# Kernel tuning notes

Hardware: AMD Instinct MI355X
Metric: run time of the kernel (lower is better)

Reference implementation:

```python
import jax, jax.numpy as jnp
import numpy as np

GRID = 48          # static voxel-grid extent (positions generated in [0, GRID)^3)
K = 3              # kernel size per axis (odd -> offset = 0.0 in the original module)
C = (K - 1) // 2   # kernel center
VOXEL_SIZE = 1.0   # forward default in DeConvolution.call


def setup_inputs() -> dict:
    key = jax.random.key(0)
    k1, k2 = jax.random.split(key)
    g = np.arange(GRID)
    coords = np.stack(np.meshgrid(g, g, g, indexing='ij'), axis=-1).reshape(-1, 3)
    # sparse input point cloud: half-density sub-lattice; dense-ish output lattice
    inp_positions = jnp.asarray(coords[coords.sum(axis=1) % 2 == 0], jnp.float32)  # (55296, 3)
    out_positions = jnp.asarray(coords, jnp.float32)                               # (110592, 3)
    n_in = inp_positions.shape[0]
    cin, cout = 256, 256
    features = jax.random.normal(k1, (n_in, cin), dtype=jnp.float32)
    # SparseConvTranspose kernel: [k, k, k, in_channels, filters]
    W = jax.random.normal(k2, (K, K, K, cin, cout), dtype=jnp.float32) * 0.05
    return {"features": features, "inp_positions": inp_positions,
            "out_positions": out_positions, "W": W}


def reference(features, inp_positions, out_positions, W):
    # Voxelize. kernel is odd -> offset = 0.0, so v = floor(p / voxel_size).
    vin = jnp.floor(inp_positions / VOXEL_SIZE).astype(jnp.int32)   # (N_in, 3)
    vout = jnp.floor(out_positions / VOXEL_SIZE).astype(jnp.int32)  # (N_out, 3)
    n_in = features.shape[0]

    # Dense voxel -> input-row hash grid (-1 = empty voxel).
    grid = jnp.full((GRID, GRID, GRID), -1, dtype=jnp.int32)
    grid = grid.at[vin[:, 0], vin[:, 1], vin[:, 2]].set(
        jnp.arange(n_in, dtype=jnp.int32))

    out = jnp.zeros((vout.shape[0], W.shape[-1]), dtype=features.dtype)
    # Transposed sparse conv: out[j] += W[v_in - v_out + C] @ feat[i]
    # Static 27-tap loop; each tap is a gather + dense GEMM.
    for dx in range(-C, C + 1):
        for dy in range(-C, C + 1):
            for dz in range(-C, C + 1):
                u = vout + jnp.array([dx, dy, dz], dtype=jnp.int32)   # source voxel
                inb = jnp.all((u >= 0) & (u < GRID), axis=1)
                uc = jnp.clip(u, 0, GRID - 1)
                idx = grid[uc[:, 0], uc[:, 1], uc[:, 2]]              # (N_out,)
                valid = inb & (idx >= 0)
                g = jnp.where(valid[:, None],
                              features[jnp.maximum(idx, 0)], 0.0)     # (N_out, Cin)
                out = out + g @ W[dx + C, dy + C, dz + C]             # (N_out, Cout)
    return out
```

## Files before the change

kernel.cpp:

```cpp
#include <hip/hip_runtime.h>

#define NIN   55296
#define CIN   256
#define COUT  256
#define NTH   512
#define NBLK  432

typedef __attribute__((ext_vector_type(8))) _Float16 half8;
typedef __attribute__((ext_vector_type(4))) _Float16 half4;
typedef __attribute__((ext_vector_type(4))) float f32x4;

typedef const __attribute__((address_space(1))) void* gp_t;
typedef __attribute__((address_space(3))) void* lp_t;
__device__ __forceinline__ void gload16(const void* g, char* l) {
  __builtin_amdgcn_global_load_lds((gp_t)g, (lp_t)l, 16, 0, 0);
}

__global__ void k_feat_cvt(const float* __restrict__ f, _Float16* __restrict__ o, int n4) {
  int i = blockIdx.x * blockDim.x + threadIdx.x;
  if (i >= n4) return;
  f32x4 v = ((const f32x4*)f)[i];
  half4 r;
  r[0] = (_Float16)v[0]; r[1] = (_Float16)v[1];
  r[2] = (_Float16)v[2]; r[3] = (_Float16)v[3];
  ((half4*)o)[i] = r;
}

__global__ void k_w_cvt(const float* __restrict__ W, _Float16* __restrict__ Wt,
                        float* __restrict__ zeros) {
  int i = blockIdx.x * blockDim.x + threadIdx.x;
  int d   = i >> 16;
  int rem = i & 65535;
  int n   = rem >> 8;
  int k   = rem & 255;
  Wt[i] = (_Float16)W[(d << 16) + (k << 8) + n];
  if (blockIdx.x == 0 && threadIdx.x < 128) zeros[threadIdx.x] = 0.0f;
}

__global__ __launch_bounds__(NTH, 2)
void k_conv8(const _Float16* __restrict__ featb, const _Float16* __restrict__ wt,
             const char* __restrict__ zeros, float* __restrict__ out) {
  extern __shared__ char lds[];
  int* orow = (int*)(lds + 131072);

  const int braw = blockIdx.x;
  const int b    = (braw & 7) * 54 + (braw >> 3);
  const int p    = b & 1;
  const int tile = b >> 1;

  const int tid = threadIdx.x;
  const int w   = tid >> 6;
  const int l   = tid & 63;

  const int rr  = w * 16 + (l >> 2);
  const int swz = ((l & 3) ^ ((l >> 3) & 3)) * 16;

  int xs[2], ys[2], zs[2];
#pragma unroll
  for (int q = 0; q < 2; ++q) {
    int e = tile * 256 + q * 128 + rr;
    int c = e / 24;
    int zi = e - c * 24;
    int x = c / 48;
    int y = c - x * 48;
    xs[q] = x; ys[q] = y; zs[q] = 2 * zi + ((x + y + p) & 1);
  }
  const char* wtc  = (const char*)wt;
  const char* featc = (const char*)featb;
  const int bro0 = rr * 512 + swz;
  const int bro1 = (128 + rr) * 512 + swz;

  const int wm = w >> 2, wn = w & 3;
  const int lr = l & 15, kg = l >> 4;
  const int rsw = (kg ^ ((lr >> 1) & 3)) * 16;
  const int aRd = (wm * 128 + lr) * 64 + rsw;
  const int bRd = (wn * 64 + lr) * 64 + rsw;

  if (tid < 256) {
    int e = tile * 256 + tid;
    int c = e / 24;
    int zi = e - c * 24;
    int x = c / 48;
    int y = c - x * 48;
    int z = 2 * zi + ((x + y + p) & 1);
    orow[tid] = (x * 48 + y) * 48 + z;
  }

  auto offpar = [](int d) { return ((d / 9) + (d / 3) % 3 + (d % 3) + 1) & 1; };
  const char* asrc[2];
  const char* wtile;
  auto setoff = [&](int d27) {
    int dx = d27 / 9 - 1, dy = (d27 / 3) % 3 - 1, dz = d27 % 3 - 1;
#pragma unroll
    for (int q = 0; q < 2; ++q) {
      int ux = xs[q] + dx, uy = ys[q] + dy, uz = zs[q] + dz;
      bool v = (unsigned)ux < 48u && (unsigned)uy < 48u && (unsigned)uz < 48u;
      int idx = (ux * 48 + uy) * 24 + (uz >> 1);
      asrc[q] = (v ? (featc + idx * 512) : zeros) + swz;
    }
    wtile = wtc + d27 * 131072;
  };

  int pn = 0;
  while (offpar(pn) != p) ++pn;
  setoff(pn);

  gload16(asrc[0],            lds + 0     + w * 1024);
  gload16(asrc[1],            lds + 8192  + w * 1024);
  gload16(wtile + bro0,       lds + 32768 + w * 1024);
  gload16(wtile + bro1,       lds + 40960 + w * 1024);
  gload16(asrc[0] + 64,       lds + 16384 + w * 1024);
  gload16(asrc[1] + 64,       lds + 24576 + w * 1024);
  gload16(wtile + bro0 + 64,  lds + 49152 + w * 1024);
  gload16(wtile + bro1 + 64,  lds + 57344 + w * 1024);

  asm volatile("s_waitcnt lgkmcnt(0)" ::: "memory");
  asm volatile("s_waitcnt vmcnt(4)" ::: "memory");
  __builtin_amdgcn_s_barrier();

  f32x4 acc[8][4];
#pragma unroll
  for (int i = 0; i < 8; ++i)
#pragma unroll
    for (int j = 0; j < 4; ++j) acc[i][j] = (f32x4)0.0f;

  const int S = p ? 56 : 52;

#define VMC(pfv) do { if (pfv) asm volatile("s_waitcnt vmcnt(4)" ::: "memory"); \
                      else     asm volatile("s_waitcnt vmcnt(0)" ::: "memory"); } while (0)
#define PH_MID() do { __builtin_amdgcn_s_barrier(); \
                      asm volatile("s_waitcnt lgkmcnt(0)" ::: "memory"); \
                      __builtin_amdgcn_sched_barrier(0); \
                      __builtin_amdgcn_s_setprio(1); } while (0)
#define PH_END() do { __builtin_amdgcn_s_setprio(0); \
                      __builtin_amdgcn_s_barrier(); } while (0)

  for (int s = 0; s < S; ++s) {
    const int d = s & 1;
    const char* Ab = lds + d * 65536;
    const char* Bb = Ab + 32768;
    char* Nb = lds + ((d ^ 1) * 65536);
    const int  sn  = s + 1;
    const bool pf  = sn < S;
    const int  kcn = sn & 3;
    if (pf && kcn == 0) {
      do { ++pn; } while (offpar(pn) != p);
      setoff(pn);
    }
    const int kb = kcn * 128;

    half8 a0[8], a1[8], bb0, bb1;

#pragma unroll
    for (int mf = 0; mf < 8; ++mf) a0[mf] = *(const half8*)(Ab + aRd + mf * 1024);
    bb0 = *(const half8*)(Bb + bRd);
    bb1 = *(const half8*)(Bb + bRd + 1024);
    if (pf) {
      gload16(asrc[0] + kb, Nb + 0    + w * 1024);
      gload16(asrc[1] + kb, Nb + 8192 + w * 1024);
    }
    VMC(pf);
    PH_MID();
#pragma unroll
    for (int mf = 0; mf < 8; ++mf) {
      acc[mf][0] = __builtin_amdgcn_mfma_f32_16x16x32_f16(a0[mf], bb0, acc[mf][0], 0, 0, 0);
      acc[mf][1] = __builtin_amdgcn_mfma_f32_16x16x32_f16(a0[mf], bb1, acc[mf][1], 0, 0, 0);
    }
    PH_END();

    bb0 = *(const half8*)(Bb + bRd + 2048);
    bb1 = *(const half8*)(Bb + bRd + 3072);
    if (pf) {
      gload16(wtile + bro0 + kb, Nb + 32768 + w * 1024);
      gload16(wtile + bro1 + kb, Nb + 40960 + w * 1024);
    }
    VMC(pf);
    PH_MID();
#pragma unroll
    for (int mf = 0; mf < 8; ++mf) {
      acc[mf][2] = __builtin_amdgcn_mfma_f32_16x16x32_f16(a0[mf], bb0, acc[mf][2], 0, 0, 0);
      acc[mf][3] = __builtin_amdgcn_mfma_f32_16x16x32_f16(a0[mf], bb1, acc[mf][3], 0, 0, 0);
    }
    PH_END();

#pragma unroll
    for (int mf = 0; mf < 8; ++mf) a1[mf] = *(const half8*)(Ab + 16384 + aRd + mf * 1024);
    bb0 = *(const half8*)(Bb + 16384 + bRd);
    bb1 = *(const half8*)(Bb + 16384 + bRd + 1024);
    if (pf) {
      gload16(asrc[0] + kb + 64, Nb + 16384 + w * 1024);
      gload16(asrc[1] + kb + 64, Nb + 24576 + w * 1024);
    }
    VMC(pf);
    PH_MID();
#pragma unroll
    for (int mf = 0; mf < 8; ++mf) {
      acc[mf][0] = __builtin_amdgcn_mfma_f32_16x16x32_f16(a1[mf], bb0, acc[mf][0], 0, 0, 0);
      acc[mf][1] = __builtin_amdgcn_mfma_f32_16x16x32_f16(a1[mf], bb1, acc[mf][1], 0, 0, 0);
    }
    PH_END();

    bb0 = *(const half8*)(Bb + 16384 + bRd + 2048);
    bb1 = *(const half8*)(Bb + 16384 + bRd + 3072);
    if (pf) {
      gload16(wtile + bro0 + kb + 64, Nb + 49152 + w * 1024);
      gload16(wtile + bro1 + kb + 64, Nb + 57344 + w * 1024);
    }
    VMC(pf);
    PH_MID();
#pragma unroll
    for (int mf = 0; mf < 8; ++mf) {
      acc[mf][2] = __builtin_amdgcn_mfma_f32_16x16x32_f16(a1[mf], bb0, acc[mf][2], 0, 0, 0);
      acc[mf][3] = __builtin_amdgcn_mfma_f32_16x16x32_f16(a1[mf], bb1, acc[mf][3], 0, 0, 0);
    }
    PH_END();
  }

#undef VMC
#undef PH_MID
#undef PH_END

#pragma unroll
  for (int mf = 0; mf < 8; ++mf) {
#pragma unroll
    for (int i = 0; i < 4; ++i) {
      int r = wm * 128 + mf * 16 + kg * 4 + i;
      int o = orow[r];
      float* dst = out + (size_t)o * COUT + wn * 64 + lr;
#pragma unroll
      for (int nf = 0; nf < 4; ++nf) dst[nf * 16] = acc[mf][nf][i];
    }
  }
}

extern "C" void kernel_launch(void* const* d_in, const int* in_sizes, int n_in,
                              void* d_out, int out_size, void* d_ws, size_t ws_size,
                              hipStream_t stream) {
  const float* features = (const float*)d_in[0];
  const float* W = (const float*)d_in[3];
  float* out = (float*)d_out;

  char* ws = (char*)d_ws;
  _Float16* featb = (_Float16*)ws;
  _Float16* Wt    = (_Float16*)(ws + 28311552);
  float*    zeros = (float*)(ws + 28311552 + 3538944);

  (void)hipFuncSetAttribute(reinterpret_cast<const void*>(k_conv8),
                            hipFuncAttributeMaxDynamicSharedMemorySize, 132096);

  {
    int n4 = NIN * CIN / 4;
    k_feat_cvt<<<(n4 + 255) / 256, 256, 0, stream>>>(features, featb, n4);
  }
  k_w_cvt<<<27 * 65536 / 256, 256, 0, stream>>>(W, Wt, zeros);

  k_conv8<<<NBLK, NTH, 132096, stream>>>(featb, Wt, (const char*)zeros, out);
}
```

Measured before the change: 236.0 us.

## Collapse four-phase barriered main loop into one sync per K-step

Replaces the four sub-phase loop, which had a barrier, an explicit vmcnt wait and a priority toggle per phase, with a single __syncthreads per K-step. Each step first reads all A and B fragments for the double-buffered stage into registers. It then issues all eight global-to-LDS prefetches for the next stage and runs 64 MFMAs back to back. It also replaces the parity-search loop for the next kernel offset with a fixed stride of 2. The aim is to cut barrier and wait overhead and give the matrix units a longer uninterrupted burst. In exchange it holds more fragment registers live, which could limit occupancy or cause spills, and each step now waits for all of the previous step's loads at once.

```diff
diff --git a/kernel.cpp b/kernel.cpp
--- a/kernel.cpp
+++ b/kernel.cpp
@@ -65,7 +65,7 @@
     int y = c - x * 48;
     xs[q] = x; ys[q] = y; zs[q] = 2 * zi + ((x + y + p) & 1);
   }
-  const char* wtc  = (const char*)wt;
+  const char* wtc   = (const char*)wt;
   const char* featc = (const char*)featb;
   const int bro0 = rr * 512 + swz;
   const int bro1 = (128 + rr) * 512 + swz;
@@ -86,7 +86,6 @@
     orow[tid] = (x * 48 + y) * 48 + z;
   }
 
-  auto offpar = [](int d) { return ((d / 9) + (d / 3) % 3 + (d % 3) + 1) & 1; };
   const char* asrc[2];
   const char* wtile;
   auto setoff = [&](int d27) {
@@ -101,23 +100,18 @@
     wtile = wtc + d27 * 131072;
   };
 
-  int pn = 0;
-  while (offpar(pn) != p) ++pn;
+  int pn = p ? 0 : 1;
   setoff(pn);
 
   gload16(asrc[0],            lds + 0     + w * 1024);
   gload16(asrc[1],            lds + 8192  + w * 1024);
+  gload16(asrc[0] + 64,       lds + 16384 + w * 1024);
+  gload16(asrc[1] + 64,       lds + 24576 + w * 1024);
   gload16(wtile + bro0,       lds + 32768 + w * 1024);
   gload16(wtile + bro1,       lds + 40960 + w * 1024);
-  gload16(asrc[0] + 64,       lds + 16384 + w * 1024);
-  gload16(asrc[1] + 64,       lds + 24576 + w * 1024);
   gload16(wtile + bro0 + 64,  lds + 49152 + w * 1024);
   gload16(wtile + bro1 + 64,  lds + 57344 + w * 1024);
 
-  asm volatile("s_waitcnt lgkmcnt(0)" ::: "memory");
-  asm volatile("s_waitcnt vmcnt(4)" ::: "memory");
-  __builtin_amdgcn_s_barrier();
-
   f32x4 acc[8][4];
 #pragma unroll
   for (int i = 0; i < 8; ++i)
@@ -126,99 +120,50 @@
 
   const int S = p ? 56 : 52;
 
-#define VMC(pfv) do { if (pfv) asm volatile("s_waitcnt vmcnt(4)" ::: "memory"); \
-                      else     asm volatile("s_waitcnt vmcnt(0)" ::: "memory"); } while (0)
-#define PH_MID() do { __builtin_amdgcn_s_barrier(); \
-                      asm volatile("s_waitcnt lgkmcnt(0)" ::: "memory"); \
-                      __builtin_amdgcn_sched_barrier(0); \
-                      __builtin_amdgcn_s_setprio(1); } while (0)
-#define PH_END() do { __builtin_amdgcn_s_setprio(0); \
-                      __builtin_amdgcn_s_barrier(); } while (0)
-
   for (int s = 0; s < S; ++s) {
-    const int d = s & 1;
-    const char* Ab = lds + d * 65536;
-    const char* Bb = Ab + 32768;
-    char* Nb = lds + ((d ^ 1) * 65536);
-    const int  sn  = s + 1;
-    const bool pf  = sn < S;
-    const int  kcn = sn & 3;
-    if (pf && kcn == 0) {
-      do { ++pn; } while (offpar(pn) != p);
-      setoff(pn);
+    __syncthreads();
+
+    const char* Ab = lds + (s & 1) * 65536;
+
+    half8 a0[8], a1[8], b0[4], b1[4];
+#pragma unroll
+    for (int nf = 0; nf < 4; ++nf) b0[nf] = *(const half8*)(Ab + 32768 + bRd + nf * 1024);
+#pragma unroll
+    for (int mf = 0; mf < 8; ++mf) a0[mf] = *(const half8*)(Ab + aRd + mf * 1024);
+#pragma unroll
+    for (int nf = 0; nf < 4; ++nf) b1[nf] = *(const half8*)(Ab + 49152 + bRd + nf * 1024);
+#pragma unroll
+    for (int mf = 0; mf < 8; ++mf) a1[mf] = *(const half8*)(Ab + 16384 + aRd + mf * 1024);
+
+    const int sn = s + 1;
+    if (sn < S) {
+      if ((sn & 3) == 0) { pn += 2; setoff(pn); }
+      char* Nb = lds + (sn & 1) * 65536;
+      const int kb = (sn & 3) * 128;
+      gload16(asrc[0] + kb,            Nb + 0     + w * 1024);
+      gload16(asrc[1] + kb,            Nb + 8192  + w * 1024);
+      gload16(asrc[0] + kb + 64,       Nb + 16384 + w * 1024);
+      gload16(asrc[1] + kb + 64,       Nb + 24576 + w * 1024);
+      gload16(wtile + bro0 + kb,       Nb + 32768 + w * 1024);
+      gload16(wtile + bro1 + kb,       Nb + 40960 + w * 1024);
+      gload16(wtile + bro0 + kb + 64,  Nb + 49152 + w * 1024);
+      gload16(wtile + bro1 + kb + 64,  Nb + 57344 + w * 1024);
     }
-    const int kb = kcn * 128;
-
-    half8 a0[8], a1[8], bb0, bb1;
-
-#pragma unroll
-    for (int mf = 0; mf < 8; ++mf) a0[mf] = *(const half8*)(Ab + aRd + mf * 1024);
-    bb0 = *(const half8*)(Bb + bRd);
-    bb1 = *(const half8*)(Bb + bRd + 1024);
-    if (pf) {
-      gload16(asrc[0] + kb, Nb + 0    + w * 1024);
-      gload16(asrc[1] + kb, Nb + 8192 + w * 1024);
-    }
-    VMC(pf);
-    PH_MID();
-#pragma unroll
-    for (int mf = 0; mf < 8; ++mf) {
-      acc[mf][0] = __builtin_amdgcn_mfma_f32_16x16x32_f16(a0[mf], bb0, acc[mf][0], 0, 0, 0);
-      acc[mf][1] = __builtin_amdgcn_mfma_f32_16x16x32_f16(a0[mf], bb1, acc[mf][1], 0, 0, 0);
-    }
-    PH_END();
-
-    bb0 = *(const half8*)(Bb + bRd + 2048);
-    bb1 = *(const half8*)(Bb + bRd + 3072);
-    if (pf) {
-      gload16(wtile + bro0 + kb, Nb + 32768 + w * 1024);
-      gload16(wtile + bro1 + kb, Nb + 40960 + w * 1024);
-    }
-    VMC(pf);
-    PH_MID();
-#pragma unroll
-    for (int mf = 0; mf < 8; ++mf) {
-      acc[mf][2] = __builtin_amdgcn_mfma_f32_16x16x32_f16(a0[mf], bb0, acc[mf][2], 0, 0, 0);
-      acc[mf][3] = __builtin_amdgcn_mfma_f32_16x16x32_f16(a0[mf], bb1, acc[mf][3], 0, 0, 0);
-    }
-    PH_END();
-
-#pragma unroll
-    for (int mf = 0; mf < 8; ++mf) a1[mf] = *(const half8*)(Ab + 16384 + aRd + mf * 1024);
-    bb0 = *(const half8*)(Bb + 16384 + bRd);
-    bb1 = *(const half8*)(Bb + 16384 + bRd + 1024);
-    if (pf) {
-      gload16(asrc[0] + kb + 64, Nb + 16384 + w * 1024);
-      gload16(asrc[1] + kb + 64, Nb + 24576 + w * 1024);
-    }
-    VMC(pf);
-    PH_MID();
-#pragma unroll
-    for (int mf = 0; mf < 8; ++mf) {
-      acc[mf][0] = __builtin_amdgcn_mfma_f32_16x16x32_f16(a1[mf], bb0, acc[mf][0], 0, 0, 0);
-      acc[mf][1] = __builtin_amdgcn_mfma_f32_16x16x32_f16(a1[mf], bb1, acc[mf][1], 0, 0, 0);
-    }
-    PH_END();
-
-    bb0 = *(const half8*)(Bb + 16384 + bRd + 2048);
-    bb1 = *(const half8*)(Bb + 16384 + bRd + 3072);
-    if (pf) {
-      gload16(wtile + bro0 + kb + 64, Nb + 49152 + w * 1024);
-      gload16(wtile + bro1 + kb + 64, Nb + 57344 + w * 1024);
-    }
-    VMC(pf);
-    PH_MID();
-#pragma unroll
-    for (int mf = 0; mf < 8; ++mf) {
-      acc[mf][2] = __builtin_amdgcn_mfma_f32_16x16x32_f16(a1[mf], bb0, acc[mf][2], 0, 0, 0);
-      acc[mf][3] = __builtin_amdgcn_mfma_f32_16x16x32_f16(a1[mf], bb1, acc[mf][3], 0, 0, 0);
-    }
-    PH_END();
-  }
-
-#undef VMC
-#undef PH_MID
-#undef PH_END
+    __builtin_amdgcn_sched_barrier(0);
+
+    __builtin_amdgcn_s_setprio(1);
+#pragma unroll
+    for (int mf = 0; mf < 8; ++mf)
+#pragma unroll
+      for (int nf = 0; nf < 4; ++nf)
+        acc[mf][nf] = __builtin_amdgcn_mfma_f32_16x16x32_f16(a0[mf], b0[nf], acc[mf][nf], 0, 0, 0);
+#pragma unroll
+    for (int mf = 0; mf < 8; ++mf)
+#pragma unroll
+      for (int nf = 0; nf < 4; ++nf)
+        acc[mf][nf] = __builtin_amdgcn_mfma_f32_16x16x32_f16(a1[mf], b1[nf], acc[mf][nf], 0, 0, 0);
+    __builtin_amdgcn_s_setprio(0);
+  }
 
 #pragma unroll
   for (int mf = 0; mf < 8; ++mf) {
```

Measured after the change: 208.4 us. 1.13x faster.
